# Performance work log

Measured on AMD Instinct MI355X. Metric: run time of the kernel, lower is better.

## Reference

```python
import jax, jax.numpy as jnp
import numpy as np

HEADS = 16
DIM_HEAD = 64
QUERY_DIM = 1024
INNER_DIM = HEADS * DIM_HEAD  # 1024
SCALE = DIM_HEAD ** (-0.5)


def setup_inputs() -> dict:
    key = jax.random.key(0)
    ks = jax.random.split(key, 6)
    B, S = 4, 2048
    hidden_states = jax.random.normal(ks[0], (B, S, QUERY_DIM), dtype=jnp.float32)
    # Linear weights stored as [in, out] for x @ W convention
    init = 1.0 / np.sqrt(QUERY_DIM)
    Wq = jax.random.uniform(ks[1], (QUERY_DIM, INNER_DIM), jnp.float32, -init, init)
    Wk = jax.random.uniform(ks[2], (QUERY_DIM, INNER_DIM), jnp.float32, -init, init)
    Wv = jax.random.uniform(ks[3], (QUERY_DIM, INNER_DIM), jnp.float32, -init, init)
    Wo = jax.random.uniform(ks[4], (INNER_DIM, QUERY_DIM), jnp.float32, -init, init)
    bo = jax.random.uniform(ks[5], (QUERY_DIM,), jnp.float32, -init, init)
    return {"hidden_states": hidden_states, "Wq": Wq, "Wk": Wk, "Wv": Wv, "Wo": Wo, "bo": bo}


def reference(hidden_states, Wq, Wk, Wv, Wo, bo):
    B, S, _ = hidden_states.shape
    # Projections
    q = hidden_states @ Wq  # [B,S,inner]
    k = hidden_states @ Wk
    v = hidden_states @ Wv
    # [B, H, S, D]
    q = q.reshape(B, S, HEADS, DIM_HEAD).transpose(0, 2, 1, 3)
    k = k.reshape(B, S, HEADS, DIM_HEAD).transpose(0, 2, 1, 3)
    v = v.reshape(B, S, HEADS, DIM_HEAD).transpose(0, 2, 1, 3)
    # Attention scores and softmax (scale after matmul, as in source)
    scores = jnp.einsum('bhqd,bhkd->bhqk', q, k) * SCALE
    attn = jax.nn.softmax(scores, axis=-1)
    out = jnp.einsum('bhqk,bhkd->bhqd', attn, v)  # [B,H,S,D]
    out = out.transpose(0, 2, 1, 3).reshape(B, S, INNER_DIM)
    return out @ Wo + bo
```

## Files before the change

### kernel.cpp

```cpp
#include <hip/hip_runtime.h>
#include <stdint.h>

typedef short v8s __attribute__((ext_vector_type(8)));
typedef float v4f __attribute__((ext_vector_type(4)));
typedef unsigned int u32;
typedef unsigned short us;

#define LOG2E 1.44269504088896340736f

__device__ __forceinline__ u32 f2u(float x) {
  union { float f; u32 u; } t; t.f = x; return t.u;
}

__device__ __forceinline__ unsigned short bfr(float x) {
  u32 u = f2u(x);
  u32 r = u + 0x7FFFu + ((u >> 16) & 1u);
  return (unsigned short)(r >> 16);
}

__device__ __forceinline__ u32 pk2(float a, float b) {
  return __builtin_amdgcn_perm(f2u(b) + 0x8000u, f2u(a) + 0x8000u, 0x07060302u);
}

__device__ __forceinline__ void async16(const void* g, void* l) {
  __builtin_amdgcn_global_load_lds(
      (const __attribute__((address_space(1))) u32*)g,
      (__attribute__((address_space(3))) u32*)l, 16, 0, 0);
}

#define MFMA_K32(A, B, C) __builtin_amdgcn_mfma_f32_16x16x32_bf16((A), (B), (C), 0, 0, 0)

__global__ void cast_h_kernel(const float4* __restrict__ in, ushort4* __restrict__ out, int n4) {
  int i = blockIdx.x * blockDim.x + threadIdx.x;
  if (i < n4) {
    float4 v = in[i];
    ushort4 o;
    o.x = bfr(v.x); o.y = bfr(v.y); o.z = bfr(v.z); o.w = bfr(v.w);
    out[i] = o;
  }
}

__global__ void transpose_cast4_kernel(const float* __restrict__ W0, const float* __restrict__ W1,
                                       const float* __restrict__ W2, const float* __restrict__ W3,
                                       us* __restrict__ O0, us* __restrict__ O1,
                                       us* __restrict__ O2, us* __restrict__ O3) {
  __shared__ float tile[32][33];
  const int z = blockIdx.z;
  const float* in = (z == 0) ? W0 : (z == 1) ? W1 : (z == 2) ? W2 : W3;
  us* out = (z == 0) ? O0 : (z == 1) ? O1 : (z == 2) ? O2 : O3;
  const float scale = (z == 0) ? 0.125f * LOG2E : 1.0f;
  const int N = 1024;
  int n0 = blockIdx.x * 32, k0 = blockIdx.y * 32;
  int tx = threadIdx.x, ty = threadIdx.y;
#pragma unroll
  for (int j = 0; j < 32; j += 8)
    tile[ty + j][tx] = in[(size_t)(k0 + ty + j) * N + n0 + tx];
  __syncthreads();
#pragma unroll
  for (int j = 0; j < 32; j += 8)
    out[(size_t)(n0 + ty + j) * 1024 + k0 + tx] = bfr(tile[tx][ty + j] * scale);
}

template <int MODE>
__global__ __launch_bounds__(256)
void gemm_bt_kernel(const us* __restrict__ A, const us* __restrict__ Bt,
                    us* __restrict__ dQ, us* __restrict__ dK, us* __restrict__ dV,
                    float* __restrict__ outF, const float* __restrict__ bias) {
  __shared__ __align__(16) us sm[MODE == 3 ? 128 * 132 : 8192];
  us* As = sm;
  us* Bs = sm + 4096;
  const int tid = threadIdx.x;
  const int wid = tid >> 6;
  const int lane = tid & 63;
  const int quad = lane >> 4;
  const int l16 = lane & 15;
  const int tile_m = blockIdx.y * 128;
  const int tile_n = blockIdx.x * 128;
  const bool vpath = (MODE == 3) && (tile_n >= 2048);

  const int srow = wid * 32 + (lane >> 2);
  const int scol = (lane & 3) * 8;
  const us* ag = A + (size_t)(tile_m + srow) * 1024 + scol;
  const us* bg = Bt + (size_t)(tile_n + srow) * 1024 + scol;
  us* al = &As[srow * 32 + scol];
  us* bl = &Bs[srow * 32 + scol];

  v4f zero = {0.f, 0.f, 0.f, 0.f};
  v4f acc[4][4];
#pragma unroll
  for (int i = 0; i < 4; ++i)
#pragma unroll
    for (int j = 0; j < 4; ++j) acc[i][j] = zero;

  const int wm = (wid >> 1) * 64;
  const int wn = (wid & 1) * 64;

  for (int k0 = 0; k0 < 1024; k0 += 32) {
    async16(ag + k0, al);
    async16(ag + k0 + 16 * 1024, al + 16 * 32);
    async16(bg + k0, bl);
    async16(bg + k0 + 16 * 1024, bl + 16 * 32);
    __syncthreads();
    v8s a[4], b[4];
#pragma unroll
    for (int i = 0; i < 4; ++i)
      a[i] = *(const v8s*)&As[(wm + i * 16 + l16) * 32 + quad * 8];
#pragma unroll
    for (int j = 0; j < 4; ++j)
      b[j] = *(const v8s*)&Bs[(wn + j * 16 + l16) * 32 + quad * 8];
    if (vpath) {
#pragma unroll
      for (int i = 0; i < 4; ++i)
#pragma unroll
        for (int j = 0; j < 4; ++j)
          acc[i][j] = MFMA_K32(a[i], b[j], acc[i][j]);
    } else {
#pragma unroll
      for (int i = 0; i < 4; ++i)
#pragma unroll
        for (int j = 0; j < 4; ++j)
          acc[i][j] = MFMA_K32(b[j], a[i], acc[i][j]);
    }
    __syncthreads();
  }

  if (MODE == 2) {
#pragma unroll
    for (int i = 0; i < 4; ++i) {
      int row = tile_m + wm + i * 16 + l16;
#pragma unroll
      for (int j = 0; j < 4; ++j) {
        int col = tile_n + wn + j * 16 + quad * 4;
        float4 bv = *(const float4*)&bias[col];
        float4 o;
        o.x = acc[i][j][0] + bv.x; o.y = acc[i][j][1] + bv.y;
        o.z = acc[i][j][2] + bv.z; o.w = acc[i][j][3] + bv.w;
        *(float4*)&outF[(size_t)row * 1024 + col] = o;
      }
    }
  } else if (!vpath) {
    us* base = (tile_n < 1024) ? dQ : dK;
    const int coln = tile_n & 1023;
#pragma unroll
    for (int i = 0; i < 4; ++i) {
      int row = tile_m + wm + i * 16 + l16;
      int b_ = row >> 11, s_ = row & 2047;
#pragma unroll
      for (int j = 0; j < 4; ++j) {
        int col = coln + wn + j * 16 + quad * 4;
        int h = (col >> 6) & 15, d = col & 63;
        uint2 pk = make_uint2(pk2(acc[i][j][0], acc[i][j][1]), pk2(acc[i][j][2], acc[i][j][3]));
        *(uint2*)&base[((size_t)(b_ * 16 + h) * 2048 + s_) * 64 + d] = pk;
      }
    }
  } else {
    const int vn = tile_n - 2048;
#pragma unroll
    for (int i = 0; i < 4; ++i) {
      int sp = wm + (i >> 1) * 32 + quad * 8 + (i & 1) * 4;
#pragma unroll
      for (int j = 0; j < 4; ++j) {
        int col = wn + j * 16 + l16;
        uint2 pk = make_uint2(pk2(acc[i][j][0], acc[i][j][1]), pk2(acc[i][j][2], acc[i][j][3]));
        *(uint2*)&sm[col * 132 + sp] = pk;
      }
    }
    __syncthreads();
    const int b_ = tile_m >> 11;
    const int sbase = tile_m & 2047;
#pragma unroll
    for (int it = 0; it < 8; ++it) {
      int u = it * 256 + tid;
      int col = u >> 4, sp = (u & 15) * 8;
      v8s val = *(const v8s*)&sm[col * 132 + sp];
      int colg = vn + col;
      int h = (colg >> 6) & 15, d = colg & 63;
      *(v8s*)&dV[((size_t)(b_ * 16 + h) * 64 + d) * 2048 + sbase + sp] = val;
    }
  }
}

__global__ __launch_bounds__(256, 3)
void flash_kernel(const us* __restrict__ Q, const us* __restrict__ K,
                  const us* __restrict__ Vt, us* __restrict__ O) {
  __shared__ __align__(16) us Ks[128 * 64];
  __shared__ __align__(16) us Vts[64 * 128];

  const int tid = threadIdx.x;
  const int wid = tid >> 6;
  const int lane = tid & 63;
  const int quad = lane >> 4;
  const int l16 = lane & 15;
  const int bh = blockIdx.y;
  const int q0 = blockIdx.x * 128;
  const int wq = wid * 32;
  const us* Qp = Q + (size_t)bh * (2048 * 64);
  const us* Kp = K + (size_t)bh * (2048 * 64);
  const us* Vp = Vt + (size_t)bh * (64 * 2048);

  v8s qB[2][2];
#pragma unroll
  for (int mi = 0; mi < 2; ++mi)
#pragma unroll
    for (int ks = 0; ks < 2; ++ks)
      qB[mi][ks] = *(const v8s*)&Qp[(size_t)(q0 + wq + mi * 16 + l16) * 64 + ks * 32 + quad * 8];

  v4f zero = {0.f, 0.f, 0.f, 0.f};
  v4f o[4][2];
#pragma unroll
  for (int i = 0; i < 4; ++i)
#pragma unroll
    for (int mi = 0; mi < 2; ++mi) o[i][mi] = zero;
  float l_st[2] = {0.f, 0.f};
  const float MSUB = 8.0f * LOG2E;

  for (int kv0 = 0; kv0 < 2048; kv0 += 128) {
    __syncthreads();
    {
      int r0 = wid * 32 + (lane >> 3);
      int c = lane & 7;
#pragma unroll
      for (int it = 0; it < 4; ++it) {
        int rr = r0 + it * 8;
        int cg = c ^ (rr & 7);
        async16(Kp + (size_t)(kv0 + rr) * 64 + cg * 8, &Ks[rr * 64 + c * 8]);
      }
    }
    {
      int d0 = wid * 16 + (lane >> 4);
      int c = lane & 15;
#pragma unroll
      for (int it = 0; it < 4; ++it) {
        int dd = d0 + it * 4;
        int cg = c ^ (dd & 15);
        async16(Vp + (size_t)dd * 2048 + kv0 + cg * 8, &Vts[dd * 128 + c * 8]);
      }
    }
    __syncthreads();

#pragma unroll
    for (int hf = 0; hf < 2; ++hf) {
      v4f sT[4][2];
#pragma unroll
      for (int m = 0; m < 4; ++m)
#pragma unroll
        for (int mi = 0; mi < 2; ++mi) sT[m][mi] = zero;
#pragma unroll
      for (int ks = 0; ks < 2; ++ks) {
        v8s kA[4];
#pragma unroll
        for (int m = 0; m < 4; ++m) {
          int kvr = hf * 64 + m * 16 + l16;
          int cc = (ks * 4 + quad) ^ (l16 & 7);
          kA[m] = *(const v8s*)&Ks[kvr * 64 + cc * 8];
        }
#pragma unroll
        for (int m = 0; m < 4; ++m)
#pragma unroll
          for (int mi = 0; mi < 2; ++mi)
            sT[m][mi] = MFMA_K32(kA[m], qB[mi][ks], sT[m][mi]);
      }

#pragma unroll
      for (int cp = 0; cp < 2; ++cp) {
        v8s bp[2];
#pragma unroll
        for (int mi = 0; mi < 2; ++mi) {
          union { u32 w[4]; v8s s; } u;
#pragma unroll
          for (int dm = 0; dm < 2; ++dm) {
            int m = cp * 2 + dm;
            float p0 = __builtin_amdgcn_exp2f(sT[m][mi][0] - MSUB);
            float p1 = __builtin_amdgcn_exp2f(sT[m][mi][1] - MSUB);
            float p2 = __builtin_amdgcn_exp2f(sT[m][mi][2] - MSUB);
            float p3 = __builtin_amdgcn_exp2f(sT[m][mi][3] - MSUB);
            l_st[mi] += (p0 + p1) + (p2 + p3);
            u.w[dm * 2] = pk2(p0, p1);
            u.w[dm * 2 + 1] = pk2(p2, p3);
          }
          bp[mi] = u.s;
        }
#pragma unroll
        for (int i = 0; i < 4; ++i) {
          int d = i * 16 + l16;
          int cc = (hf * 8 + cp * 4 + quad) ^ l16;
          v8s vt = *(const v8s*)&Vts[d * 128 + cc * 8];
#pragma unroll
          for (int mi = 0; mi < 2; ++mi)
            o[i][mi] = MFMA_K32(vt, bp[mi], o[i][mi]);
        }
      }
    }
  }

#pragma unroll
  for (int mi = 0; mi < 2; ++mi) {
    float l = l_st[mi];
    l += __shfl_xor(l, 16);
    l += __shfl_xor(l, 32);
    l_st[mi] = 1.0f / l;
  }

  __syncthreads();
#pragma unroll
  for (int mi = 0; mi < 2; ++mi) {
    int q = wq + mi * 16 + l16;
#pragma unroll
    for (int i = 0; i < 4; ++i)
#pragma unroll
      for (int rp = 0; rp < 4; rp += 2) {
        int d = i * 16 + quad * 4 + rp;
        u32 pk = pk2(o[i][mi][rp] * l_st[mi], o[i][mi][rp + 1] * l_st[mi]);
        *(u32*)&Ks[q * 64 + ((d >> 3) ^ (q & 7)) * 8 + (d & 7)] = pk;
      }
  }
  __syncthreads();
  const int b_ = bh >> 4, h_ = bh & 15;
#pragma unroll
  for (int it = 0; it < 4; ++it) {
    int u = it * 256 + tid;
    int row = u >> 3, ch = u & 7;
    v8s val = *(const v8s*)&Ks[row * 64 + (ch ^ (row & 7)) * 8];
    *(v8s*)&O[((size_t)(b_ * 2048 + q0 + row)) * 1024 + h_ * 64 + ch * 8] = val;
  }
}

extern "C" void kernel_launch(void* const* d_in, const int* in_sizes, int n_in,
                              void* d_out, int out_size, void* d_ws, size_t ws_size,
                              hipStream_t stream) {
  const float* Hs = (const float*)d_in[0];
  const float* Wq = (const float*)d_in[1];
  const float* Wk = (const float*)d_in[2];
  const float* Wv = (const float*)d_in[3];
  const float* Wo = (const float*)d_in[4];
  const float* bo = (const float*)d_in[5];
  float* out = (float*)d_out;
  char* ws = (char*)d_ws;
  const size_t MiB = 1ull << 20;
  us* Hb  = (us*)(ws);
  us* Wqt = (us*)(ws + 16 * MiB);
  us* Wkt = (us*)(ws + 18 * MiB);
  us* Wvt = (us*)(ws + 20 * MiB);
  us* Wot = (us*)(ws + 22 * MiB);
  us* Qb  = (us*)(ws + 24 * MiB);
  us* Kb  = (us*)(ws + 40 * MiB);
  us* Vtb = (us*)(ws + 56 * MiB);
  us* Ob  = Hb;
  (void)Wkt; (void)Wvt;

  cast_h_kernel<<<8192, 256, 0, stream>>>((const float4*)Hs, (ushort4*)Hb, 2097152);
  transpose_cast4_kernel<<<dim3(32, 32, 4), dim3(32, 8), 0, stream>>>(Wq, Wk, Wv, Wo,
                                                                      Wqt, Wkt, Wvt, Wot);
  gemm_bt_kernel<3><<<dim3(24, 64), 256, 0, stream>>>(Hb, Wqt, Qb, Kb, Vtb, nullptr, nullptr);
  flash_kernel<<<dim3(16, 64), 256, 0, stream>>>(Qb, Kb, Vtb, Ob);
  gemm_bt_kernel<2><<<dim3(8, 64), 256, 0, stream>>>(Ob, Wot, nullptr, nullptr, nullptr, out, bo);
}
```

Measured before the change: 289.7 us.

## Deepen GEMM K-tile with swizzle, enlarge flash KV tile, compute row sums via MFMA

The projection GEMM now loads 64-wide K slices into an XOR-swizzled shared layout, which halves the number of barrier pairs and aims to avoid LDS bank conflicts. The flash kernel processes 256 KV rows per iteration instead of 128, with occupancy lowered from 3 to 2 blocks to fit the doubled shared memory. Softmax denominators are now accumulated with an MFMA against a ones vector, using the bf16-rounded probabilities, instead of scalar adds and cross-lane shuffles. Larger tiles cut synchronisation but reduce occupancy and latency hiding. The MFMA row sum adds matrix work while removing VALU adds.

```diff
diff --git a/kernel.cpp b/kernel.cpp
--- a/kernel.cpp
+++ b/kernel.cpp
@@ -66,9 +66,9 @@
 void gemm_bt_kernel(const us* __restrict__ A, const us* __restrict__ Bt,
                     us* __restrict__ dQ, us* __restrict__ dK, us* __restrict__ dV,
                     float* __restrict__ outF, const float* __restrict__ bias) {
-  __shared__ __align__(16) us sm[MODE == 3 ? 128 * 132 : 8192];
+  __shared__ __align__(16) us sm[MODE == 3 ? 16896 : 16384];
   us* As = sm;
-  us* Bs = sm + 4096;
+  us* Bs = sm + 8192;
   const int tid = threadIdx.x;
   const int wid = tid >> 6;
   const int lane = tid & 63;
@@ -78,12 +78,8 @@
   const int tile_n = blockIdx.x * 128;
   const bool vpath = (MODE == 3) && (tile_n >= 2048);
 
-  const int srow = wid * 32 + (lane >> 2);
-  const int scol = (lane & 3) * 8;
-  const us* ag = A + (size_t)(tile_m + srow) * 1024 + scol;
-  const us* bg = Bt + (size_t)(tile_n + srow) * 1024 + scol;
-  us* al = &As[srow * 32 + scol];
-  us* bl = &Bs[srow * 32 + scol];
+  const int srow = wid * 32 + (lane >> 3);
+  const int sc = lane & 7;
 
   v4f zero = {0.f, 0.f, 0.f, 0.f};
   v4f acc[4][4];
@@ -95,31 +91,41 @@
   const int wm = (wid >> 1) * 64;
   const int wn = (wid & 1) * 64;
 
-  for (int k0 = 0; k0 < 1024; k0 += 32) {
-    async16(ag + k0, al);
-    async16(ag + k0 + 16 * 1024, al + 16 * 32);
-    async16(bg + k0, bl);
-    async16(bg + k0 + 16 * 1024, bl + 16 * 32);
-    __syncthreads();
-    v8s a[4], b[4];
-#pragma unroll
-    for (int i = 0; i < 4; ++i)
-      a[i] = *(const v8s*)&As[(wm + i * 16 + l16) * 32 + quad * 8];
-#pragma unroll
-    for (int j = 0; j < 4; ++j)
-      b[j] = *(const v8s*)&Bs[(wn + j * 16 + l16) * 32 + quad * 8];
-    if (vpath) {
-#pragma unroll
-      for (int i = 0; i < 4; ++i)
-#pragma unroll
-        for (int j = 0; j < 4; ++j)
-          acc[i][j] = MFMA_K32(a[i], b[j], acc[i][j]);
-    } else {
-#pragma unroll
-      for (int i = 0; i < 4; ++i)
-#pragma unroll
-        for (int j = 0; j < 4; ++j)
-          acc[i][j] = MFMA_K32(b[j], a[i], acc[i][j]);
+  for (int k0 = 0; k0 < 1024; k0 += 64) {
+#pragma unroll
+    for (int it = 0; it < 4; ++it) {
+      int rr = srow + it * 8;
+      int cg = sc ^ (rr & 7);
+      async16(A + (size_t)(tile_m + rr) * 1024 + k0 + cg * 8, &As[rr * 64 + sc * 8]);
+      async16(Bt + (size_t)(tile_n + rr) * 1024 + k0 + cg * 8, &Bs[rr * 64 + sc * 8]);
+    }
+    __syncthreads();
+#pragma unroll
+    for (int ks = 0; ks < 2; ++ks) {
+      v8s a[4], b[4];
+#pragma unroll
+      for (int i = 0; i < 4; ++i) {
+        int row = wm + i * 16 + l16;
+        a[i] = *(const v8s*)&As[row * 64 + (((ks * 4 + quad) ^ (row & 7)) * 8)];
+      }
+#pragma unroll
+      for (int j = 0; j < 4; ++j) {
+        int row = wn + j * 16 + l16;
+        b[j] = *(const v8s*)&Bs[row * 64 + (((ks * 4 + quad) ^ (row & 7)) * 8)];
+      }
+      if (vpath) {
+#pragma unroll
+        for (int i = 0; i < 4; ++i)
+#pragma unroll
+          for (int j = 0; j < 4; ++j)
+            acc[i][j] = MFMA_K32(a[i], b[j], acc[i][j]);
+      } else {
+#pragma unroll
+        for (int i = 0; i < 4; ++i)
+#pragma unroll
+          for (int j = 0; j < 4; ++j)
+            acc[i][j] = MFMA_K32(b[j], a[i], acc[i][j]);
+      }
     }
     __syncthreads();
   }
@@ -180,11 +186,11 @@
   }
 }
 
-__global__ __launch_bounds__(256, 3)
+__global__ __launch_bounds__(256, 2)
 void flash_kernel(const us* __restrict__ Q, const us* __restrict__ K,
                   const us* __restrict__ Vt, us* __restrict__ O) {
-  __shared__ __align__(16) us Ks[128 * 64];
-  __shared__ __align__(16) us Vts[64 * 128];
+  __shared__ __align__(16) us Ks[256 * 64];
+  __shared__ __align__(16) us Vts[64 * 256];
 
   const int tid = threadIdx.x;
   const int wid = tid >> 6;
@@ -211,35 +217,37 @@
   for (int i = 0; i < 4; ++i)
 #pragma unroll
     for (int mi = 0; mi < 2; ++mi) o[i][mi] = zero;
-  float l_st[2] = {0.f, 0.f};
+  v4f l_acc[2] = {zero, zero};
+  const us one_bf = 0x3F80;
+  const v8s ones = {(short)one_bf, (short)one_bf, (short)one_bf, (short)one_bf,
+                    (short)one_bf, (short)one_bf, (short)one_bf, (short)one_bf};
   const float MSUB = 8.0f * LOG2E;
 
-  for (int kv0 = 0; kv0 < 2048; kv0 += 128) {
+  for (int kv0 = 0; kv0 < 2048; kv0 += 256) {
     __syncthreads();
     {
-      int r0 = wid * 32 + (lane >> 3);
+      int r0 = wid * 64 + (lane >> 3);
       int c = lane & 7;
 #pragma unroll
-      for (int it = 0; it < 4; ++it) {
+      for (int it = 0; it < 8; ++it) {
         int rr = r0 + it * 8;
         int cg = c ^ (rr & 7);
         async16(Kp + (size_t)(kv0 + rr) * 64 + cg * 8, &Ks[rr * 64 + c * 8]);
       }
     }
     {
-      int d0 = wid * 16 + (lane >> 4);
-      int c = lane & 15;
-#pragma unroll
-      for (int it = 0; it < 4; ++it) {
-        int dd = d0 + it * 4;
-        int cg = c ^ (dd & 15);
-        async16(Vp + (size_t)dd * 2048 + kv0 + cg * 8, &Vts[dd * 128 + c * 8]);
-      }
-    }
-    __syncthreads();
-
-#pragma unroll
-    for (int hf = 0; hf < 2; ++hf) {
+      int c = lane & 31;
+#pragma unroll
+      for (int it = 0; it < 8; ++it) {
+        int dd = wid * 16 + it * 2 + (lane >> 5);
+        int cg = c ^ (dd & 31);
+        async16(Vp + (size_t)dd * 2048 + kv0 + cg * 8, &Vts[dd * 256 + c * 8]);
+      }
+    }
+    __syncthreads();
+
+#pragma unroll
+    for (int hf = 0; hf < 4; ++hf) {
       v4f sT[4][2];
 #pragma unroll
       for (int m = 0; m < 4; ++m)
@@ -274,17 +282,18 @@
             float p1 = __builtin_amdgcn_exp2f(sT[m][mi][1] - MSUB);
             float p2 = __builtin_amdgcn_exp2f(sT[m][mi][2] - MSUB);
             float p3 = __builtin_amdgcn_exp2f(sT[m][mi][3] - MSUB);
-            l_st[mi] += (p0 + p1) + (p2 + p3);
             u.w[dm * 2] = pk2(p0, p1);
             u.w[dm * 2 + 1] = pk2(p2, p3);
           }
           bp[mi] = u.s;
+          l_acc[mi] = MFMA_K32(ones, bp[mi], l_acc[mi]);
         }
+        int g = hf * 2 + cp;
 #pragma unroll
         for (int i = 0; i < 4; ++i) {
           int d = i * 16 + l16;
-          int cc = (hf * 8 + cp * 4 + quad) ^ l16;
-          v8s vt = *(const v8s*)&Vts[d * 128 + cc * 8];
+          int cc = (g * 4 + quad) ^ (d & 31);
+          v8s vt = *(const v8s*)&Vts[d * 256 + cc * 8];
 #pragma unroll
           for (int mi = 0; mi < 2; ++mi)
             o[i][mi] = MFMA_K32(vt, bp[mi], o[i][mi]);
@@ -293,13 +302,9 @@
     }
   }
 
-#pragma unroll
-  for (int mi = 0; mi < 2; ++mi) {
-    float l = l_st[mi];
-    l += __shfl_xor(l, 16);
-    l += __shfl_xor(l, 32);
-    l_st[mi] = 1.0f / l;
-  }
+  float invl[2];
+#pragma unroll
+  for (int mi = 0; mi < 2; ++mi) invl[mi] = 1.0f / l_acc[mi][0];
 
   __syncthreads();
 #pragma unroll
@@ -310,7 +315,7 @@
 #pragma unroll
       for (int rp = 0; rp < 4; rp += 2) {
         int d = i * 16 + quad * 4 + rp;
-        u32 pk = pk2(o[i][mi][rp] * l_st[mi], o[i][mi][rp + 1] * l_st[mi]);
+        u32 pk = pk2(o[i][mi][rp] * invl[mi], o[i][mi][rp + 1] * invl[mi]);
         *(u32*)&Ks[q * 64 + ((d >> 3) ^ (q & 7)) * 8 + (d & 7)] = pk;
       }
   }
```

Result: faster. 269.7 us (-6.9%).
